# Kernel tuning notes

Hardware: AMD Instinct MI355X
Metric: run time of the kernel (lower is better)

The kernel has to match this reference:

```python
import jax, jax.numpy as jnp
import numpy as np

N_NODES = 50000
N_EDGES = 640000
RANK = 128
ORDER = 3
N_GRAPHS = 50
LN_EPS = 1e-5


def setup_inputs() -> dict:
    key = jax.random.key(0)
    ks = jax.random.split(key, 8)
    features = jax.random.normal(ks[0], (N_NODES, RANK), dtype=jnp.float32)
    src = jax.random.randint(ks[1], (N_EDGES,), 0, N_NODES, dtype=jnp.int32)
    dst = jax.random.randint(ks[2], (N_EDGES,), 0, N_NODES, dtype=jnp.int32)
    batch_num_nodes = jnp.full((N_GRAPHS,), N_NODES // N_GRAPHS, dtype=jnp.int32)
    scale = 1.0 / np.sqrt(RANK)
    Ws = jax.random.normal(ks[3], (ORDER, RANK, RANK), dtype=jnp.float32) * scale
    bs = jnp.zeros((ORDER, RANK), dtype=jnp.float32)
    gammas = jnp.ones((ORDER, RANK), dtype=jnp.float32)
    betas = jnp.zeros((ORDER, RANK), dtype=jnp.float32)
    return {"features": features, "src": src, "dst": dst,
            "batch_num_nodes": batch_num_nodes,
            "Ws": Ws, "bs": bs, "gammas": gammas, "betas": betas}


def _layer_norm(x, gamma, beta):
    mu = jnp.mean(x, axis=-1, keepdims=True)
    var = jnp.mean(jnp.square(x - mu), axis=-1, keepdims=True)
    return (x - mu) * jax.lax.rsqrt(var + LN_EPS) * gamma + beta


def reference(features, src, dst, batch_num_nodes, Ws, bs, gammas, betas):
    ones = jnp.ones((src.shape[0],), dtype=features.dtype)
    deg_out = jax.ops.segment_sum(ones, src, num_segments=N_NODES)  # out-degree of src nodes
    deg_in = jax.ops.segment_sum(ones, dst, num_segments=N_NODES)   # in-degree of dst nodes
    inv_sqrt_out = jax.lax.rsqrt(jnp.maximum(deg_out, 1.0))[:, None]
    inv_sqrt_in = jax.lax.rsqrt(jnp.maximum(deg_in, 1.0))[:, None]

    feats = features
    for i in range(ORDER):
        # DGL GraphConv, norm='both': h = D_in^{-1/2} A D_out^{-1/2} (X W) + b
        h = (feats @ Ws[i]) * inv_sqrt_out
        agg = jax.ops.segment_sum(h[src], dst, num_segments=N_NODES)
        h = agg * inv_sqrt_in + bs[i]
        h = _layer_norm(h, gammas[i], betas[i])
        feats = jax.nn.relu(h)  # dropout is identity at inference

    first_idx = jnp.cumsum(jnp.concatenate([jnp.zeros((1,), jnp.int32), batch_num_nodes[:-1]]))
    return feats[first_idx]
```

## Files before the change

### kernel.cpp

```cpp
#include <hip/hip_runtime.h>

#define RANK 128
#define LN_EPS 1e-5f

#define NCH 4
#define CHUNK 12800
#define BINS (NCH * CHUNK)
#define ECH 64
#define BT 1024
#define BMWL ((BINS + 31) / 32)

using short8 = __attribute__((ext_vector_type(8))) short;
using v4f    = __attribute__((ext_vector_type(4))) float;

__device__ inline unsigned short f2bf(float f) {
    unsigned u = __float_as_uint(f);
    unsigned r = (u + 0x7FFF + ((u >> 16) & 1)) >> 16;
    return (unsigned short)r;
}

__global__ __launch_bounds__(BT) void hist_part(const int* __restrict__ src,
                                                const int* __restrict__ dst,
                                                int* __restrict__ pdst,
                                                int* __restrict__ psrc, int nE) {
    __shared__ int h[CHUNK];
    int c = blockIdx.x, n = blockIdx.y, z = blockIdx.z;
    const int* arr = z ? src : dst;
    int* pout = z ? psrc : pdst;
    int base = n * CHUNK;
    for (int i = threadIdx.x; i < CHUNK; i += BT) h[i] = 0;
    __syncthreads();
    int epc = (nE + ECH - 1) / ECH;
    int e0 = c * epc, e1 = min(e0 + epc, nE);
    for (int e = e0 + (int)threadIdx.x; e < e1; e += BT) {
        int v = arr[e] - base;
        if ((unsigned)v < (unsigned)CHUNK) atomicAdd(&h[v], 1);
    }
    __syncthreads();
    int* o = pout + (size_t)c * BINS + base;
    for (int i = threadIdx.x; i < CHUNK; i += BT) o[i] = h[i];
}

__global__ __launch_bounds__(256) void reduce_scan1(const int* __restrict__ pdst,
                                                    const int* __restrict__ psrc,
                                                    int* __restrict__ counts,
                                                    float* __restrict__ invin,
                                                    float* __restrict__ invout,
                                                    int* __restrict__ ends,
                                                    int* __restrict__ bsums, int M) {
    __shared__ int tmp[256];
    int tid = threadIdx.x;
    int gid = blockIdx.x * 256 + tid;
    int cd = 0, cs = 0;
    if (gid < M) {
#pragma unroll 8
        for (int c = 0; c < ECH; c++) {
            cd += pdst[(size_t)c * BINS + gid];
            cs += psrc[(size_t)c * BINS + gid];
        }
        counts[gid] = cd;
        invin[gid]  = rsqrtf(fmaxf((float)cd, 1.0f));
        invout[gid] = rsqrtf(fmaxf((float)cs, 1.0f));
    }
    tmp[tid] = cd;
    __syncthreads();
    for (int off = 1; off < 256; off <<= 1) {
        int t = (tid >= off) ? tmp[tid - off] : 0;
        __syncthreads();
        tmp[tid] += t;
        __syncthreads();
    }
    if (gid < M) ends[gid] = tmp[tid];
    if (tid == 255) bsums[blockIdx.x] = tmp[255];
}

__global__ __launch_bounds__(256) void scan23_offs(int* __restrict__ ends,
                                                   const int* __restrict__ counts,
                                                   const int* __restrict__ bsums,
                                                   int* __restrict__ pdst, int nb, int M) {
    __shared__ int red[256];
    int tid = threadIdx.x;
    int b = blockIdx.x;
    red[tid] = (tid < b && tid < nb) ? bsums[tid] : 0;
    __syncthreads();
    for (int off = 128; off > 0; off >>= 1) {
        if (tid < off) red[tid] += red[tid + off];
        __syncthreads();
    }
    int prefix = red[0];
    int gid = b * 256 + tid;
    if (gid < M) {
        int e = ends[gid] + prefix;
        ends[gid] = e;
        int run = e - counts[gid];
#pragma unroll 8
        for (int c = 0; c < ECH; c++) {
            size_t idx = (size_t)c * BINS + gid;
            int t = pdst[idx];
            pdst[idx] = run;
            run += t;
        }
    }
}

__global__ __launch_bounds__(BT) void fill_sorted(const int* __restrict__ src,
                                                  const int* __restrict__ dst,
                                                  const int* __restrict__ pdst,
                                                  int* __restrict__ csr_src, int nE) {
    __shared__ int cur[CHUNK];
    int c = blockIdx.x, n = blockIdx.y;
    int base = n * CHUNK;
    const int* o = pdst + (size_t)c * BINS + base;
    for (int i = threadIdx.x; i < CHUNK; i += BT) cur[i] = o[i];
    __syncthreads();
    int epc = (nE + ECH - 1) / ECH;
    int e0 = c * epc, e1 = min(e0 + epc, nE);
    for (int e = e0 + (int)threadIdx.x; e < e1; e += BT) {
        int d = dst[e] - base;
        if ((unsigned)d < (unsigned)CHUNK) {
            int pos = atomicAdd(&cur[d], 1);
            csr_src[pos] = src[e];
        }
    }
}

__global__ __launch_bounds__(256) void mark_expand3(const int* __restrict__ bnn, int nG,
                                                    const int* __restrict__ ends,
                                                    const int* __restrict__ csr_src,
                                                    int* __restrict__ T3, int* __restrict__ cnt3,
                                                    int* __restrict__ T2, int* __restrict__ cnt2) {
    __shared__ unsigned bm[BMWL];
    __shared__ int lcnt;
    int tid = threadIdx.x;
    for (int i = tid; i < BMWL; i += 256) bm[i] = 0;
    if (tid == 0) lcnt = 0;
    __syncthreads();
    if (tid < 64) {
        int lane = tid;
        if (nG <= 64) {
            int v = (lane < nG) ? bnn[lane] : 0;
            int orig = v;
#pragma unroll
            for (int off = 1; off < 64; off <<= 1) {
                int t = __shfl_up(v, off);
                if (lane >= off) v += t;
            }
            int excl = v - orig;
            if (lane < nG) T3[lane] = excl;
            if (lane == 0) *cnt3 = nG;
        } else if (lane == 0) {
            int idx = 0;
            for (int g = 0; g < nG; g++) { T3[g] = idx; idx += bnn[g]; }
            *cnt3 = nG;
        }
    }
    __syncthreads();
    int lane = tid & 63, w = tid >> 6;
    for (int i = w; i < nG; i += 4) {
        int node = T3[i];
        int end = ends[node];
        int beg = (node == 0) ? 0 : ends[node - 1];
        for (int e0 = beg; e0 < end; e0 += 64) {
            if (e0 + lane < end) {
                int u = csr_src[e0 + lane];
                unsigned old = atomicOr(&bm[u >> 5], 1u << (u & 31));
                if (!((old >> (u & 31)) & 1)) {
                    int pos = atomicAdd(&lcnt, 1);
                    T2[pos] = u;
                }
            }
        }
    }
    __syncthreads();
    if (tid == 0) *cnt2 = lcnt;
}

__global__ __launch_bounds__(256) void frontier_csr(const int* __restrict__ list,
                                                    const int* __restrict__ cnt,
                                                    const int* __restrict__ ends,
                                                    const int* __restrict__ csr_src,
                                                    unsigned* __restrict__ bm_out,
                                                    int* __restrict__ out_list,
                                                    int* __restrict__ out_cnt) {
    int lane = threadIdx.x & 63;
    int wg = blockIdx.x * 4 + (threadIdx.x >> 6);
    int nW = gridDim.x * 4;
    int n = *cnt;
    for (int i = wg; i < n; i += nW) {
        int node = list[i];
        int end = ends[node];
        int beg = (node == 0) ? 0 : ends[node - 1];
        for (int e0 = beg; e0 < end; e0 += 64) {
            int u = 0;
            bool flag = false;
            if (e0 + lane < end) {
                u = csr_src[e0 + lane];
                unsigned old = atomicOr(&bm_out[u >> 5], 1u << (u & 31));
                flag = !((old >> (u & 31)) & 1);
            }
            unsigned long long mask = __ballot(flag);
            if (mask) {
                int leader = __ffsll((long long)mask) - 1;
                int base = 0;
                if (lane == leader) base = atomicAdd(out_cnt, __popcll(mask));
                base = __shfl(base, leader);
                if (flag) out_list[base + __popcll(mask & ((1ull << lane) - 1))] = u;
            }
        }
    }
}

__global__ __launch_bounds__(256) void repack_convert(const float* __restrict__ Ws,
                                                      short* __restrict__ Wt,
                                                      const float* __restrict__ X,
                                                      const float* __restrict__ invout,
                                                      unsigned* __restrict__ Xs, int n2) {
    int bid = blockIdx.x;
    if (bid < 24) {
        int l = bid >> 3;
        int s = (bid & 7) * 256 + threadIdx.x;
        int lane = s & 63, ct = (s >> 6) & 7, k0 = s >> 9;
        int m = lane & 15, quad = lane >> 4;
        const float* W = Ws + (size_t)l * RANK * RANK;
        short* o = Wt + (size_t)l * 16384 + (size_t)s * 8;
#pragma unroll
        for (int j = 0; j < 8; j++)
            o[j] = (short)f2bf(W[(k0 * 32 + quad * 8 + j) * RANK + ct * 16 + m]);
    } else {
        int i = (bid - 24) * 256 + threadIdx.x;
        if (i < n2) {
            float s = invout[i >> 6];
            float2 v = ((const float2*)X)[i];
            Xs[i] = (unsigned)f2bf(v.x * s) | ((unsigned)f2bf(v.y * s) << 16);
        }
    }
}

template <int LAST>
__global__ __launch_bounds__(256) void layer_fused(const unsigned* __restrict__ Fin,
                                                   const int* __restrict__ ends,
                                                   const int* __restrict__ csr_src,
                                                   const short* __restrict__ Wt,
                                                   const float* __restrict__ invin,
                                                   const float* __restrict__ invout,
                                                   const float* __restrict__ bias,
                                                   const float* __restrict__ gamma,
                                                   const float* __restrict__ beta,
                                                   const int* __restrict__ list,
                                                   const int* __restrict__ cnt,
                                                   unsigned short* __restrict__ Fout,
                                                   float* __restrict__ out) {
    __shared__ short As[16][136];
    __shared__ float sstat[2][4][16];
    __shared__ float sinv[2][16];
    __shared__ int snode[16];
    int tid = threadIdx.x;
    int w = tid >> 6, lane = tid & 63;
    int seg = lane >> 4, m = lane & 15;
    int n = *cnt;
    int tiles = (n + 15) >> 4;

    float bb[2], gg[2], pp[2];
#pragma unroll
    for (int j = 0; j < 2; j++) {
        int col = (w * 2 + j) * 16 + m;
        bb[j] = bias[col]; gg[j] = gamma[col]; pp[j] = beta[col];
    }

    for (int t = blockIdx.x; t < tiles; t += gridDim.x) {
        int base = t * 16;

        for (int q = 0; q < 4; q++) {
            int rr = w * 4 + q;
            int gr = base + rr;
            float ax[8];
#pragma unroll
            for (int k = 0; k < 8; k++) ax[k] = 0.f;
            int node = -1;
            if (gr < n) {
                node = list[gr];
                int end = ends[node];
                int e = (node == 0) ? 0 : ends[node - 1];
                while (e < end) {
                    int rem = end - e;
                    int myi = 0;
                    if (lane < rem) myi = csr_src[e + lane];
                    int nn = min(rem, 64);
                    int p = 0;
                    for (; p + 16 <= nn; p += 16) {
                        uint4 u[4];
#pragma unroll
                        for (int gi = 0; gi < 4; gi++) {
                            int idx = __shfl(myi, p + gi * 4 + seg);
                            u[gi] = *(const uint4*)(Fin + (size_t)idx * 64 + m * 4);
                        }
#pragma unroll
                        for (int gi = 0; gi < 4; gi++) {
                            ax[0] += __uint_as_float(u[gi].x << 16);
                            ax[1] += __uint_as_float(u[gi].x & 0xFFFF0000u);
                            ax[2] += __uint_as_float(u[gi].y << 16);
                            ax[3] += __uint_as_float(u[gi].y & 0xFFFF0000u);
                            ax[4] += __uint_as_float(u[gi].z << 16);
                            ax[5] += __uint_as_float(u[gi].z & 0xFFFF0000u);
                            ax[6] += __uint_as_float(u[gi].w << 16);
                            ax[7] += __uint_as_float(u[gi].w & 0xFFFF0000u);
                        }
                    }
                    for (; p < nn; p += 4) {
                        bool act = (p + seg) < nn;
                        int idx = __shfl(myi, (p + seg) & 63);
                        if (act) {
                            uint4 u = *(const uint4*)(Fin + (size_t)idx * 64 + m * 4);
                            ax[0] += __uint_as_float(u.x << 16);
                            ax[1] += __uint_as_float(u.x & 0xFFFF0000u);
                            ax[2] += __uint_as_float(u.y << 16);
                            ax[3] += __uint_as_float(u.y & 0xFFFF0000u);
                            ax[4] += __uint_as_float(u.z << 16);
                            ax[5] += __uint_as_float(u.z & 0xFFFF0000u);
                            ax[6] += __uint_as_float(u.w << 16);
                            ax[7] += __uint_as_float(u.w & 0xFFFF0000u);
                        }
                    }
                    e += nn;
                }
#pragma unroll
                for (int k = 0; k < 8; k++) {
                    ax[k] += __shfl_xor(ax[k], 16);
                    ax[k] += __shfl_xor(ax[k], 32);
                }
            }
            if (seg == 0) {
                uint4 o;
                o.x = (unsigned)f2bf(ax[0]) | ((unsigned)f2bf(ax[1]) << 16);
                o.y = (unsigned)f2bf(ax[2]) | ((unsigned)f2bf(ax[3]) << 16);
                o.z = (unsigned)f2bf(ax[4]) | ((unsigned)f2bf(ax[5]) << 16);
                o.w = (unsigned)f2bf(ax[6]) | ((unsigned)f2bf(ax[7]) << 16);
                *(uint4*)&As[rr][8 * m] = o;
            }
            if (lane == 0) {
                snode[rr] = node;
                sinv[0][rr] = (node >= 0) ? invin[node] : 1.f;
                sinv[1][rr] = (node >= 0) ? invout[node] : 1.f;
            }
        }
        __syncthreads();

        short8 a[4];
#pragma unroll
        for (int k0 = 0; k0 < 4; k0++)
            a[k0] = *(const short8*)&As[m][k0 * 32 + seg * 8];
        v4f acc[2];
        acc[0] = (v4f){0.f, 0.f, 0.f, 0.f};
        acc[1] = (v4f){0.f, 0.f, 0.f, 0.f};
#pragma unroll
        for (int k0 = 0; k0 < 4; k0++) {
#pragma unroll
            for (int j = 0; j < 2; j++) {
                int ct = w * 2 + j;
                short8 b = *(const short8*)(Wt + (size_t)((k0 * 8 + ct) * 64 + lane) * 8);
                acc[j] = __builtin_amdgcn_mfma_f32_16x16x32_bf16(a[k0], b, acc[j], 0, 0, 0);
            }
        }

        float x[4][2];
#pragma unroll
        for (int r = 0; r < 4; r++) {
            int row = seg * 4 + r;
            float iv = sinv[0][row];
            float s = 0.f, sq = 0.f;
#pragma unroll
            for (int j = 0; j < 2; j++) {
                float c = acc[j][r] * iv + bb[j];
                x[r][j] = c;
                s += c; sq += c * c;
            }
#pragma unroll
            for (int off = 1; off < 16; off <<= 1) {
                s  += __shfl_xor(s, off);
                sq += __shfl_xor(sq, off);
            }
            if (m == 0) { sstat[0][w][row] = s; sstat[1][w][row] = sq; }
        }
        __syncthreads();

#pragma unroll
        for (int r = 0; r < 4; r++) {
            int row = seg * 4 + r;
            int gr = base + row;
            if (gr >= n) continue;
            float s  = sstat[0][0][row] + sstat[0][1][row] + sstat[0][2][row] + sstat[0][3][row];
            float sq = sstat[1][0][row] + sstat[1][1][row] + sstat[1][2][row] + sstat[1][3][row];
            float mu = s * (1.0f / RANK);
            float var = sq * (1.0f / RANK) - mu * mu;
            float rs = rsqrtf(var + LN_EPS);
#pragma unroll
            for (int j = 0; j < 2; j++) {
                int col = (w * 2 + j) * 16 + m;
                float y = fmaxf((x[r][j] - mu) * rs * gg[j] + pp[j], 0.f);
                if (LAST) {
                    out[(size_t)gr * RANK + col] = y;
                } else {
                    Fout[(size_t)snode[row] * RANK + col] = f2bf(y * sinv[1][row]);
                }
            }
        }
        __syncthreads();
    }
}

extern "C" void kernel_launch(void* const* d_in, const int* in_sizes, int n_in,
                              void* d_out, int out_size, void* d_ws, size_t ws_size,
                              hipStream_t stream) {
    const float* features = (const float*)d_in[0];
    const int* src = (const int*)d_in[1];
    const int* dst = (const int*)d_in[2];
    const int* bnn = (const int*)d_in[3];
    const float* Ws = (const float*)d_in[4];
    const float* bs = (const float*)d_in[5];
    const float* gammas = (const float*)d_in[6];
    const float* betas = (const float*)d_in[7];
    float* out = (float*)d_out;

    int M  = in_sizes[0] / RANK;
    int nE = in_sizes[1];
    int nG = in_sizes[3];
    int bmw = (M + 31) / 32;

    char* ws = (char*)d_ws;
    size_t off = 0;
    auto alloc = [&](size_t bytes) {
        void* p = ws + off;
        off += (bytes + 255) & ~(size_t)255;
        return p;
    };
    int*   counts  = (int*)alloc((size_t)M * 4);
    int*   ends    = (int*)alloc((size_t)M * 4);
    int*   bsums   = (int*)alloc(256 * 4);
    float* invout  = (float*)alloc((size_t)M * 4);
    float* invin   = (float*)alloc((size_t)M * 4);
    int*   csr_src = (int*)alloc((size_t)nE * 4);
    short* Wt      = (short*)alloc((size_t)3 * 16384 * 2);
    short* Xs      = (short*)alloc((size_t)M * RANK * 2);
    short* F1      = (short*)alloc((size_t)M * RANK * 2);
    short* F2      = (short*)alloc((size_t)M * RANK * 2);
    int*   pdst    = (int*)alloc((size_t)ECH * BINS * 4);
    int*   psrc    = (int*)alloc((size_t)ECH * BINS * 4);
    char*  zbase   = (char*)alloc((size_t)(bmw + 1) * 4);
    unsigned* bm1  = (unsigned*)zbase;
    int*   cnt1    = (int*)(bm1 + bmw);
    int*   cnt2    = (int*)alloc(256);
    int*   cnt3    = (int*)alloc(256);
    int*   T3      = (int*)alloc((size_t)((nG + 63) & ~63) * 4);
    int*   T2      = (int*)alloc((size_t)M * 4);
    int*   T1      = (int*)alloc((size_t)M * 4);

    int nb = (M + 255) / 256;

    hipMemsetAsync(zbase, 0, (size_t)(bmw + 1) * 4, stream);

    hist_part<<<dim3(ECH, NCH, 2), BT, 0, stream>>>(src, dst, pdst, psrc, nE);
    reduce_scan1<<<nb, 256, 0, stream>>>(pdst, psrc, counts, invin, invout, ends, bsums, M);
    scan23_offs<<<nb, 256, 0, stream>>>(ends, counts, bsums, pdst, nb, M);
    fill_sorted<<<dim3(ECH, NCH), BT, 0, stream>>>(src, dst, pdst, csr_src, nE);

    mark_expand3<<<1, 256, 0, stream>>>(bnn, nG, ends, csr_src, T3, cnt3, T2, cnt2);
    frontier_csr<<<64, 256, 0, stream>>>(T2, cnt2, ends, csr_src, bm1, T1, cnt1);

    int cb = (M * 64 + 255) / 256;
    repack_convert<<<24 + cb, 256, 0, stream>>>(Ws, Wt, features, invout, (unsigned*)Xs, M * 64);

    layer_fused<0><<<512, 256, 0, stream>>>((const unsigned*)Xs, ends, csr_src, Wt,
                                            invin, invout, bs, gammas, betas,
                                            T1, cnt1, (unsigned short*)F1, nullptr);
    layer_fused<0><<<64, 256, 0, stream>>>((const unsigned*)F1, ends, csr_src, Wt + 16384,
                                           invin, invout, bs + RANK, gammas + RANK, betas + RANK,
                                           T2, cnt2, (unsigned short*)F2, nullptr);
    layer_fused<1><<<(nG + 15) / 16, 256, 0, stream>>>((const unsigned*)F2, ends, csr_src, Wt + 32768,
                                                       invin, invout, bs + 2 * RANK,
                                                       gammas + 2 * RANK, betas + 2 * RANK,
                                                       T3, cnt3, nullptr, out);
}
```

Measured before the change: 191.4 us.

## Drop bf16 feature pre-conversion, gather fp32 directly; fold weight repack into histogram

```diff
diff --git a/kernel.cpp b/kernel.cpp
--- a/kernel.cpp
+++ b/kernel.cpp
@@ -21,28 +21,62 @@
 
 __global__ __launch_bounds__(BT) void hist_part(const int* __restrict__ src,
                                                 const int* __restrict__ dst,
-                                                int* __restrict__ pdst,
-                                                int* __restrict__ psrc, int nE) {
+                                                unsigned short* __restrict__ pdst,
+                                                unsigned short* __restrict__ psrc,
+                                                const float* __restrict__ Ws,
+                                                short* __restrict__ Wt, int nE) {
+    int c = blockIdx.x, n = blockIdx.y, z = blockIdx.z;
+    if (c == ECH) {
+        int sid = (n + 4 * z) * BT + threadIdx.x;
+        if (sid < 3 * 2048) {
+            int l = sid >> 11;
+            int s = sid & 2047;
+            int lane = s & 63, ct = (s >> 6) & 7, k0 = s >> 9;
+            int m = lane & 15, quad = lane >> 4;
+            const float* W = Ws + (size_t)l * RANK * RANK;
+            short* o = Wt + (size_t)l * 16384 + (size_t)s * 8;
+#pragma unroll
+            for (int j = 0; j < 8; j++)
+                o[j] = (short)f2bf(W[(k0 * 32 + quad * 8 + j) * RANK + ct * 16 + m]);
+        }
+        return;
+    }
     __shared__ int h[CHUNK];
-    int c = blockIdx.x, n = blockIdx.y, z = blockIdx.z;
     const int* arr = z ? src : dst;
-    int* pout = z ? psrc : pdst;
+    unsigned short* pout = z ? psrc : pdst;
     int base = n * CHUNK;
     for (int i = threadIdx.x; i < CHUNK; i += BT) h[i] = 0;
     __syncthreads();
     int epc = (nE + ECH - 1) / ECH;
     int e0 = c * epc, e1 = min(e0 + epc, nE);
-    for (int e = e0 + (int)threadIdx.x; e < e1; e += BT) {
-        int v = arr[e] - base;
+    int tid = threadIdx.x;
+    int a0 = min((e0 + 3) & ~3, e1);
+    if (tid < a0 - e0) {
+        int v = arr[e0 + tid] - base;
         if ((unsigned)v < (unsigned)CHUNK) atomicAdd(&h[v], 1);
     }
-    __syncthreads();
-    int* o = pout + (size_t)c * BINS + base;
-    for (int i = threadIdx.x; i < CHUNK; i += BT) o[i] = h[i];
-}
-
-__global__ __launch_bounds__(256) void reduce_scan1(const int* __restrict__ pdst,
-                                                    const int* __restrict__ psrc,
+    int rem = e1 - a0;
+    int nv = (rem > 0) ? (rem & ~3) : 0;
+    for (int e = a0 + tid * 4; e < a0 + nv; e += BT * 4) {
+        int4 v4 = *(const int4*)(arr + e);
+        int v;
+        v = v4.x - base; if ((unsigned)v < (unsigned)CHUNK) atomicAdd(&h[v], 1);
+        v = v4.y - base; if ((unsigned)v < (unsigned)CHUNK) atomicAdd(&h[v], 1);
+        v = v4.z - base; if ((unsigned)v < (unsigned)CHUNK) atomicAdd(&h[v], 1);
+        v = v4.w - base; if ((unsigned)v < (unsigned)CHUNK) atomicAdd(&h[v], 1);
+    }
+    int t0 = a0 + nv;
+    if (tid < e1 - t0) {
+        int v = arr[t0 + tid] - base;
+        if ((unsigned)v < (unsigned)CHUNK) atomicAdd(&h[v], 1);
+    }
+    __syncthreads();
+    unsigned short* o = pout + (size_t)c * BINS + base;
+    for (int i = threadIdx.x; i < CHUNK; i += BT) o[i] = (unsigned short)h[i];
+}
+
+__global__ __launch_bounds__(256) void reduce_scan1(const unsigned short* __restrict__ pdst,
+                                                    const unsigned short* __restrict__ psrc,
                                                     int* __restrict__ counts,
                                                     float* __restrict__ invin,
                                                     float* __restrict__ invout,
@@ -77,7 +111,8 @@
 __global__ __launch_bounds__(256) void scan23_offs(int* __restrict__ ends,
                                                    const int* __restrict__ counts,
                                                    const int* __restrict__ bsums,
-                                                   int* __restrict__ pdst, int nb, int M) {
+                                                   const unsigned short* __restrict__ pdst,
+                                                   int* __restrict__ pcur, int nb, int M) {
     __shared__ int red[256];
     int tid = threadIdx.x;
     int b = blockIdx.x;
@@ -97,7 +132,7 @@
         for (int c = 0; c < ECH; c++) {
             size_t idx = (size_t)c * BINS + gid;
             int t = pdst[idx];
-            pdst[idx] = run;
+            pcur[idx] = run;
             run += t;
         }
     }
@@ -105,22 +140,39 @@
 
 __global__ __launch_bounds__(BT) void fill_sorted(const int* __restrict__ src,
                                                   const int* __restrict__ dst,
-                                                  const int* __restrict__ pdst,
+                                                  const int* __restrict__ pcur,
                                                   int* __restrict__ csr_src, int nE) {
     __shared__ int cur[CHUNK];
     int c = blockIdx.x, n = blockIdx.y;
     int base = n * CHUNK;
-    const int* o = pdst + (size_t)c * BINS + base;
+    const int* o = pcur + (size_t)c * BINS + base;
     for (int i = threadIdx.x; i < CHUNK; i += BT) cur[i] = o[i];
     __syncthreads();
     int epc = (nE + ECH - 1) / ECH;
     int e0 = c * epc, e1 = min(e0 + epc, nE);
-    for (int e = e0 + (int)threadIdx.x; e < e1; e += BT) {
+    int tid = threadIdx.x;
+    int a0 = min((e0 + 3) & ~3, e1);
+    if (tid < a0 - e0) {
+        int e = e0 + tid;
         int d = dst[e] - base;
-        if ((unsigned)d < (unsigned)CHUNK) {
-            int pos = atomicAdd(&cur[d], 1);
-            csr_src[pos] = src[e];
-        }
+        if ((unsigned)d < (unsigned)CHUNK) csr_src[atomicAdd(&cur[d], 1)] = src[e];
+    }
+    int rem = e1 - a0;
+    int nv = (rem > 0) ? (rem & ~3) : 0;
+    for (int e = a0 + tid * 4; e < a0 + nv; e += BT * 4) {
+        int4 d4 = *(const int4*)(dst + e);
+        int4 s4 = *(const int4*)(src + e);
+        int d;
+        d = d4.x - base; if ((unsigned)d < (unsigned)CHUNK) csr_src[atomicAdd(&cur[d], 1)] = s4.x;
+        d = d4.y - base; if ((unsigned)d < (unsigned)CHUNK) csr_src[atomicAdd(&cur[d], 1)] = s4.y;
+        d = d4.z - base; if ((unsigned)d < (unsigned)CHUNK) csr_src[atomicAdd(&cur[d], 1)] = s4.z;
+        d = d4.w - base; if ((unsigned)d < (unsigned)CHUNK) csr_src[atomicAdd(&cur[d], 1)] = s4.w;
+    }
+    int t0 = a0 + nv;
+    if (tid < e1 - t0) {
+        int e = t0 + tid;
+        int d = dst[e] - base;
+        if ((unsigned)d < (unsigned)CHUNK) csr_src[atomicAdd(&cur[d], 1)] = src[e];
     }
 }
 
@@ -210,34 +262,9 @@
     }
 }
 
-__global__ __launch_bounds__(256) void repack_convert(const float* __restrict__ Ws,
-                                                      short* __restrict__ Wt,
-                                                      const float* __restrict__ X,
-                                                      const float* __restrict__ invout,
-                                                      unsigned* __restrict__ Xs, int n2) {
-    int bid = blockIdx.x;
-    if (bid < 24) {
-        int l = bid >> 3;
-        int s = (bid & 7) * 256 + threadIdx.x;
-        int lane = s & 63, ct = (s >> 6) & 7, k0 = s >> 9;
-        int m = lane & 15, quad = lane >> 4;
-        const float* W = Ws + (size_t)l * RANK * RANK;
-        short* o = Wt + (size_t)l * 16384 + (size_t)s * 8;
-#pragma unroll
-        for (int j = 0; j < 8; j++)
-            o[j] = (short)f2bf(W[(k0 * 32 + quad * 8 + j) * RANK + ct * 16 + m]);
-    } else {
-        int i = (bid - 24) * 256 + threadIdx.x;
-        if (i < n2) {
-            float s = invout[i >> 6];
-            float2 v = ((const float2*)X)[i];
-            Xs[i] = (unsigned)f2bf(v.x * s) | ((unsigned)f2bf(v.y * s) << 16);
-        }
-    }
-}
-
-template <int LAST>
-__global__ __launch_bounds__(256) void layer_fused(const unsigned* __restrict__ Fin,
+template <int LAST, int FP32IN>
+__global__ __launch_bounds__(256) void layer_fused(const void* __restrict__ FinV,
+                                                   const float* __restrict__ edge_scale,
                                                    const int* __restrict__ ends,
                                                    const int* __restrict__ csr_src,
                                                    const short* __restrict__ Wt,
@@ -250,6 +277,8 @@
                                                    const int* __restrict__ cnt,
                                                    unsigned short* __restrict__ Fout,
                                                    float* __restrict__ out) {
+    const unsigned* Fb = (const unsigned*)FinV;
+    const float4*  Ff = (const float4*)FinV;
     __shared__ short As[16][136];
     __shared__ float sstat[2][4][16];
     __shared__ float sinv[2][16];
@@ -288,37 +317,65 @@
                     int nn = min(rem, 64);
                     int p = 0;
                     for (; p + 16 <= nn; p += 16) {
-                        uint4 u[4];
-#pragma unroll
-                        for (int gi = 0; gi < 4; gi++) {
-                            int idx = __shfl(myi, p + gi * 4 + seg);
-                            u[gi] = *(const uint4*)(Fin + (size_t)idx * 64 + m * 4);
-                        }
-#pragma unroll
-                        for (int gi = 0; gi < 4; gi++) {
-                            ax[0] += __uint_as_float(u[gi].x << 16);
-                            ax[1] += __uint_as_float(u[gi].x & 0xFFFF0000u);
-                            ax[2] += __uint_as_float(u[gi].y << 16);
-                            ax[3] += __uint_as_float(u[gi].y & 0xFFFF0000u);
-                            ax[4] += __uint_as_float(u[gi].z << 16);
-                            ax[5] += __uint_as_float(u[gi].z & 0xFFFF0000u);
-                            ax[6] += __uint_as_float(u[gi].w << 16);
-                            ax[7] += __uint_as_float(u[gi].w & 0xFFFF0000u);
+                        if (FP32IN) {
+                            float4 fa[4], fb4[4]; float so[4];
+#pragma unroll
+                            for (int gi = 0; gi < 4; gi++) {
+                                int idx = __shfl(myi, p + gi * 4 + seg);
+                                so[gi] = edge_scale[idx];
+                                const float4* qq = Ff + (size_t)idx * 32 + m * 2;
+                                fa[gi] = qq[0]; fb4[gi] = qq[1];
+                            }
+#pragma unroll
+                            for (int gi = 0; gi < 4; gi++) {
+                                ax[0] += fa[gi].x * so[gi]; ax[1] += fa[gi].y * so[gi];
+                                ax[2] += fa[gi].z * so[gi]; ax[3] += fa[gi].w * so[gi];
+                                ax[4] += fb4[gi].x * so[gi]; ax[5] += fb4[gi].y * so[gi];
+                                ax[6] += fb4[gi].z * so[gi]; ax[7] += fb4[gi].w * so[gi];
+                            }
+                        } else {
+                            uint4 u[4];
+#pragma unroll
+                            for (int gi = 0; gi < 4; gi++) {
+                                int idx = __shfl(myi, p + gi * 4 + seg);
+                                u[gi] = *(const uint4*)(Fb + (size_t)idx * 64 + m * 4);
+                            }
+#pragma unroll
+                            for (int gi = 0; gi < 4; gi++) {
+                                ax[0] += __uint_as_float(u[gi].x << 16);
+                                ax[1] += __uint_as_float(u[gi].x & 0xFFFF0000u);
+                                ax[2] += __uint_as_float(u[gi].y << 16);
+                                ax[3] += __uint_as_float(u[gi].y & 0xFFFF0000u);
+                                ax[4] += __uint_as_float(u[gi].z << 16);
+                                ax[5] += __uint_as_float(u[gi].z & 0xFFFF0000u);
+                                ax[6] += __uint_as_float(u[gi].w << 16);
+                                ax[7] += __uint_as_float(u[gi].w & 0xFFFF0000u);
+                            }
                         }
                     }
                     for (; p < nn; p += 4) {
                         bool act = (p + seg) < nn;
                         int idx = __shfl(myi, (p + seg) & 63);
                         if (act) {
-                            uint4 u = *(const uint4*)(Fin + (size_t)idx * 64 + m * 4);
-                            ax[0] += __uint_as_float(u.x << 16);
-                            ax[1] += __uint_as_float(u.x & 0xFFFF0000u);
-                            ax[2] += __uint_as_float(u.y << 16);
-                            ax[3] += __uint_as_float(u.y & 0xFFFF0000u);
-                            ax[4] += __uint_as_float(u.z << 16);
-                            ax[5] += __uint_as_float(u.z & 0xFFFF0000u);
-                            ax[6] += __uint_as_float(u.w << 16);
-                            ax[7] += __uint_as_float(u.w & 0xFFFF0000u);
+                            if (FP32IN) {
+                                float so = edge_scale[idx];
+                                const float4* qq = Ff + (size_t)idx * 32 + m * 2;
+                                float4 fa = qq[0], fb4 = qq[1];
+                                ax[0] += fa.x * so; ax[1] += fa.y * so;
+                                ax[2] += fa.z * so; ax[3] += fa.w * so;
+                                ax[4] += fb4.x * so; ax[5] += fb4.y * so;
+                                ax[6] += fb4.z * so; ax[7] += fb4.w * so;
+                            } else {
+                                uint4 u = *(const uint4*)(Fb + (size_t)idx * 64 + m * 4);
+                                ax[0] += __uint_as_float(u.x << 16);
+                                ax[1] += __uint_as_float(u.x & 0xFFFF0000u);
+                                ax[2] += __uint_as_float(u.y << 16);
+                                ax[3] += __uint_as_float(u.y & 0xFFFF0000u);
+                                ax[4] += __uint_as_float(u.z << 16);
+                                ax[5] += __uint_as_float(u.z & 0xFFFF0000u);
+                                ax[6] += __uint_as_float(u.w << 16);
+                                ax[7] += __uint_as_float(u.w & 0xFFFF0000u);
+                            }
                         }
                     }
                     e += nn;
@@ -440,11 +497,11 @@
     float* invin   = (float*)alloc((size_t)M * 4);
     int*   csr_src = (int*)alloc((size_t)nE * 4);
     short* Wt      = (short*)alloc((size_t)3 * 16384 * 2);
-    short* Xs      = (short*)alloc((size_t)M * RANK * 2);
     short* F1      = (short*)alloc((size_t)M * RANK * 2);
     short* F2      = (short*)alloc((size_t)M * RANK * 2);
-    int*   pdst    = (int*)alloc((size_t)ECH * BINS * 4);
-    int*   psrc    = (int*)alloc((size_t)ECH * BINS * 4);
+    unsigned short* pdst = (unsigned short*)alloc((size_t)ECH * BINS * 2);
+    unsigned short* psrc = (unsigned short*)alloc((size_t)ECH * BINS * 2);
+    int*   pcur    = (int*)alloc((size_t)ECH * BINS * 4);
     char*  zbase   = (char*)alloc((size_t)(bmw + 1) * 4);
     unsigned* bm1  = (unsigned*)zbase;
     int*   cnt1    = (int*)(bm1 + bmw);
@@ -458,25 +515,22 @@
 
     hipMemsetAsync(zbase, 0, (size_t)(bmw + 1) * 4, stream);
 
-    hist_part<<<dim3(ECH, NCH, 2), BT, 0, stream>>>(src, dst, pdst, psrc, nE);
+    hist_part<<<dim3(ECH + 1, NCH, 2), BT, 0, stream>>>(src, dst, pdst, psrc, Ws, Wt, nE);
     reduce_scan1<<<nb, 256, 0, stream>>>(pdst, psrc, counts, invin, invout, ends, bsums, M);
-    scan23_offs<<<nb, 256, 0, stream>>>(ends, counts, bsums, pdst, nb, M);
-    fill_sorted<<<dim3(ECH, NCH), BT, 0, stream>>>(src, dst, pdst, csr_src, nE);
+    scan23_offs<<<nb, 256, 0, stream>>>(ends, counts, bsums, pdst, pcur, nb, M);
+    fill_sorted<<<dim3(ECH, NCH), BT, 0, stream>>>(src, dst, pcur, csr_src, nE);
 
     mark_expand3<<<1, 256, 0, stream>>>(bnn, nG, ends, csr_src, T3, cnt3, T2, cnt2);
     frontier_csr<<<64, 256, 0, stream>>>(T2, cnt2, ends, csr_src, bm1, T1, cnt1);
 
-    int cb = (M * 64 + 255) / 256;
-    repack_convert<<<24 + cb, 256, 0, stream>>>(Ws, Wt, features, invout, (unsigned*)Xs, M * 64);
-
-    layer_fused<0><<<512, 256, 0, stream>>>((const unsigned*)Xs, ends, csr_src, Wt,
-                                            invin, invout, bs, gammas, betas,
-                                            T1, cnt1, (unsigned short*)F1, nullptr);
-    layer_fused<0><<<64, 256, 0, stream>>>((const unsigned*)F1, ends, csr_src, Wt + 16384,
-                                           invin, invout, bs + RANK, gammas + RANK, betas + RANK,
-                                           T2, cnt2, (unsigned short*)F2, nullptr);
-    layer_fused<1><<<(nG + 15) / 16, 256, 0, stream>>>((const unsigned*)F2, ends, csr_src, Wt + 32768,
-                                                       invin, invout, bs + 2 * RANK,
-                                                       gammas + 2 * RANK, betas + 2 * RANK,
-                                                       T3, cnt3, nullptr, out);
-}
+    layer_fused<0, 1><<<512, 256, 0, stream>>>(features, invout, ends, csr_src, Wt,
+                                               invin, invout, bs, gammas, betas,
+                                               T1, cnt1, (unsigned short*)F1, nullptr);
+    layer_fused<0, 0><<<64, 256, 0, stream>>>(F1, nullptr, ends, csr_src, Wt + 16384,
+                                              invin, invout, bs + RANK, gammas + RANK, betas + RANK,
+                                              T2, cnt2, (unsigned short*)F2, nullptr);
+    layer_fused<1, 0><<<(nG + 15) / 16, 256, 0, stream>>>(F2, nullptr, ends, csr_src, Wt + 32768,
+                                                          invin, invout, bs + 2 * RANK,
+                                                          gammas + 2 * RANK, betas + 2 * RANK,
+                                                          T3, cnt3, nullptr, out);
+}
```

After: 178.1 us. -6.9%, faster.
